# Performance work log

Hardware: AMD Instinct MI355X
Metric: run time of the kernel (lower is better)

## Reference

```python
import jax, jax.numpy as jnp
import numpy as np
import math

VOCAB = 32000
D = 256          # d_model
SLOTS = 128      # num_slots
RANK = 32        # bilinear_rank
STEPS = 6        # max_reasoning_steps
SEQ = 512
B = 4
LN_EPS = 1e-5


def _layernorm(x, gamma, beta):
    mu = jnp.mean(x, axis=-1, keepdims=True)
    var = jnp.var(x, axis=-1, keepdims=True)
    return (x - mu) * jax.lax.rsqrt(var + LN_EPS) * gamma + beta


def setup_inputs() -> dict:
    key = jax.random.key(0)
    ks = jax.random.split(key, 16)
    # orthogonal slots H: Q,_ = qr(randn(d, num_slots)); H = Q.T  (num_slots <= d_model)
    rng = np.random.RandomState(0)
    Q, _ = np.linalg.qr(rng.randn(D, SLOTS).astype(np.float32))
    H = jnp.asarray(Q.T)  # [SLOTS, D]

    input_ids = jax.random.randint(ks[0], (B, SEQ), 0, VOCAB)
    attention_mask = jnp.ones((B, SEQ), dtype=jnp.int32)

    tok_emb = jax.random.normal(ks[1], (VOCAB, D), jnp.float32) * 0.02
    tok_emb = tok_emb.at[0].set(0.0)  # padding_idx=0
    pos_emb = jax.random.normal(ks[2], (SEQ, D), jnp.float32) * 0.02

    std_bi = math.sqrt(2.0 / (D + RANK))
    W_source = jax.random.normal(ks[3], (SLOTS, SLOTS, D, RANK), jnp.float32) * std_bi
    W_target = jax.random.normal(ks[4], (SLOTS, SLOTS, RANK, D), jnp.float32) * std_bi

    lim = math.sqrt(6.0 / (D + D))  # xavier_uniform for the square linears
    def lin(k):
        return jax.random.uniform(k, (D, D), jnp.float32, -lim, lim)  # torch Linear weight [out,in]
    wq_in, wk_slots, wv_in = lin(ks[5]), lin(ks[6]), lin(ks[7])
    wq_out, wk_fin, wv_fin = lin(ks[8]), lin(ks[9]), lin(ks[10])
    w_out = jax.random.normal(ks[11], (VOCAB, D), jnp.float32) * 0.02

    ln_gamma = jnp.ones((STEPS, D), jnp.float32)
    ln_beta = jnp.zeros((STEPS, D), jnp.float32)

    return {
        "input_ids": input_ids, "attention_mask": attention_mask,
        "tok_emb": tok_emb, "pos_emb": pos_emb, "H": H,
        "W_source": W_source, "W_target": W_target,
        "wq_in": wq_in, "wk_slots": wk_slots, "wv_in": wv_in,
        "wq_out": wq_out, "wk_fin": wk_fin, "wv_fin": wv_fin,
        "w_out": w_out, "ln_gamma": ln_gamma, "ln_beta": ln_beta,
    }


def reference(input_ids, attention_mask, tok_emb, pos_emb, H, W_source, W_target,
              wq_in, wk_slots, wv_in, wq_out, wk_fin, wv_fin, w_out,
              ln_gamma, ln_beta):
    scale = 1.0 / math.sqrt(D)
    x = tok_emb[input_ids] + pos_emb[None, :input_ids.shape[1], :]  # [B,S,D] (dropout = eval no-op)

    # input -> slot compression cross-attention
    Qi = x @ wq_in.T                     # [B,S,D]
    K_slots = H @ wk_slots.T             # [SLOTS,D]
    Vi = x @ wv_in.T                     # [B,S,D]
    A = jax.nn.softmax(jnp.einsum('bsd,kd->bsk', Qi, K_slots) * scale, axis=-1)
    m = attention_mask[:, :, None].astype(A.dtype)
    A = A * m
    A = A / (A.sum(axis=1, keepdims=True) + 1e-8)
    IR = jnp.einsum('bsk,bsd->bkd', A, Vi)    # [B,SLOTS,D]
    Hs = H[None] + IR                          # [B,SLOTS,D]

    # bilinear all-pairs slot mixing, i != j, fused as one batched contraction
    pair_mask = 1.0 - jnp.eye(SLOTS, dtype=Hs.dtype)  # [SLOTS,SLOTS]
    for step in range(STEPS):
        inter = jnp.einsum('bid,ijdr->bijr', Hs, W_source) * pair_mask[None, :, :, None]
        influence = jnp.einsum('bijr,ijrd->bjd', inter, W_target)  # [B,SLOTS,D]
        Hs = Hs + jax.nn.relu(influence)
        Hs = _layernorm(Hs, ln_gamma[step], ln_beta[step])
        # convergence break omitted: step_update norms never fall below 0.01 with these scales

    # slot -> output expansion cross-attention
    Qo = x @ wq_out.T                          # [B,S,D]
    Kf = Hs @ wk_fin.T                         # [B,SLOTS,D]
    Vf = Hs @ wv_fin.T                         # [B,SLOTS,D]
    Ae = jax.nn.softmax(jnp.einsum('bsd,bkd->bsk', Qo, Kf) * scale, axis=-1)
    Y = jnp.einsum('bsk,bkd->bsd', Ae, Vf)
    logits = Y @ w_out.T                       # [B,S,VOCAB]
    return logits
```

## Files before the change

### kernel.cpp

```cpp
#include <hip/hip_runtime.h>

typedef unsigned short u16;
typedef unsigned long long u64;
typedef short short8_t __attribute__((ext_vector_type(8)));
typedef float f32x4 __attribute__((ext_vector_type(4)));

#define SL 128
#define DM 256
#define RK 32
#define SEQ 512
#define NB 4
#define NCHUNK 32

__device__ __forceinline__ float bf2f(u16 u) {
  return __uint_as_float(((unsigned int)u) << 16);
}
__device__ __forceinline__ u16 f2bf(float f) {
  unsigned int x = __float_as_uint(f);
  x += 0x7fffu + ((x >> 16) & 1u);
  return (u16)(x >> 16);
}

__global__ __launch_bounds__(256) void cvt_k(const float* __restrict__ in,
                                             u16* __restrict__ out, int n4) {
  for (int i = blockIdx.x * blockDim.x + threadIdx.x; i < n4;
       i += gridDim.x * blockDim.x) {
    float4 v = ((const float4*)in)[i];
    u16 o0 = f2bf(v.x), o1 = f2bf(v.y), o2 = f2bf(v.z), o3 = f2bf(v.w);
    unsigned int lo = (unsigned int)o0 | ((unsigned int)o1 << 16);
    unsigned int hi = (unsigned int)o2 | ((unsigned int)o3 << 16);
    ((uint2*)out)[i] = make_uint2(lo, hi);
  }
}

struct CvtJobs { const float* src[7]; };
__global__ __launch_bounds__(256) void cvt_all_k(CvtJobs jobs,
    u16* __restrict__ wbase, u16* __restrict__ Hbf) {
  int z = blockIdx.y;
  const float* in = jobs.src[z];
  u16* out = (z < 6) ? (wbase + (size_t)z * 65536) : Hbf;
  int n4 = (z < 6) ? 16384 : 8192;
  for (int i = blockIdx.x * 256 + threadIdx.x; i < n4; i += gridDim.x * 256) {
    float4 v = ((const float4*)in)[i];
    unsigned int lo = (unsigned)f2bf(v.x) | ((unsigned)f2bf(v.y) << 16);
    unsigned int hi = (unsigned)f2bf(v.z) | ((unsigned)f2bf(v.w) << 16);
    ((uint2*)out)[i] = make_uint2(lo, hi);
  }
}

__global__ __launch_bounds__(256) void embed_k(const int* __restrict__ ids,
    const float* __restrict__ tok, const float* __restrict__ pos,
    u16* __restrict__ xbf) {
  int bs = blockIdx.x, d = threadIdx.x;
  int id = ids[bs];
  int s = bs & (SEQ - 1);
  float v = tok[(size_t)id * DM + d] + pos[(size_t)s * DM + d];
  xbf[(size_t)bs * DM + d] = f2bf(v);
}

__global__ __launch_bounds__(256) void gemm_nt(const u16* __restrict__ A,
    const u16* __restrict__ Bw, float* __restrict__ Cout, int N) {
  __shared__ u16 s_a[64 * 256];
  __shared__ u16 s_b[64 * 256];
  int tid = threadIdx.x;
  int m0 = blockIdx.x * 64, n0 = blockIdx.y * 64;
  for (int c = tid; c < 2048; c += 256) {
    int row = c >> 5;
    int ec = (c & 31) << 3;
    short8_t va = *(const short8_t*)(A + (size_t)(m0 + row) * 256 + ec);
    short8_t vb = *(const short8_t*)(Bw + (size_t)(n0 + row) * 256 + ec);
    int sw = ec ^ ((row & 7) << 3);
    *(short8_t*)(&s_a[row * 256 + sw]) = va;
    *(short8_t*)(&s_b[row * 256 + sw]) = vb;
  }
  __syncthreads();
  int lane = tid & 63;
  int w = tid >> 6;
  int wm = (w >> 1) * 32, wn = (w & 1) * 32;
  int lr = lane & 15, lk = (lane >> 4) << 3;
  f32x4 acc00 = {0.f, 0.f, 0.f, 0.f};
  f32x4 acc01 = {0.f, 0.f, 0.f, 0.f};
  f32x4 acc10 = {0.f, 0.f, 0.f, 0.f};
  f32x4 acc11 = {0.f, 0.f, 0.f, 0.f};
#pragma unroll
  for (int ks = 0; ks < 8; ++ks) {
    int ke = ks * 32 + lk;
    int r0 = wm + lr, r1 = wm + 16 + lr;
    int c0 = wn + lr, c1 = wn + 16 + lr;
    short8_t a0 = *(const short8_t*)(&s_a[r0 * 256 + (ke ^ ((r0 & 7) << 3))]);
    short8_t a1 = *(const short8_t*)(&s_a[r1 * 256 + (ke ^ ((r1 & 7) << 3))]);
    short8_t b0 = *(const short8_t*)(&s_b[c0 * 256 + (ke ^ ((c0 & 7) << 3))]);
    short8_t b1 = *(const short8_t*)(&s_b[c1 * 256 + (ke ^ ((c1 & 7) << 3))]);
    acc00 = __builtin_amdgcn_mfma_f32_16x16x32_bf16(a0, b0, acc00, 0, 0, 0);
    acc01 = __builtin_amdgcn_mfma_f32_16x16x32_bf16(a0, b1, acc01, 0, 0, 0);
    acc10 = __builtin_amdgcn_mfma_f32_16x16x32_bf16(a1, b0, acc10, 0, 0, 0);
    acc11 = __builtin_amdgcn_mfma_f32_16x16x32_bf16(a1, b1, acc11, 0, 0, 0);
  }
  int rbase = (lane >> 4) << 2;
#pragma unroll
  for (int i = 0; i < 2; ++i) {
#pragma unroll
    for (int jj = 0; jj < 2; ++jj) {
      f32x4 v = (i == 0) ? (jj == 0 ? acc00 : acc01)
                         : (jj == 0 ? acc10 : acc11);
      int row0 = m0 + wm + i * 16 + rbase;
      int col = n0 + wn + jj * 16 + lr;
#pragma unroll
      for (int q = 0; q < 4; ++q)
        Cout[(size_t)(row0 + q) * (size_t)N + col] = v[q];
    }
  }
}

__global__ __launch_bounds__(256) void gemm_nt3(const u16* __restrict__ A,
    const u16* __restrict__ wbase, float* __restrict__ Cbase, int q0, int q1,
    int q2, size_t cstride) {
  int z = blockIdx.z;
  int q = (z == 0) ? q0 : ((z == 1) ? q1 : q2);
  const u16* Bw = wbase + (size_t)q * 65536;
  float* Cout = Cbase + (size_t)z * cstride;
  __shared__ u16 s_a[64 * 256];
  __shared__ u16 s_b[64 * 256];
  int tid = threadIdx.x;
  int m0 = blockIdx.x * 64, n0 = blockIdx.y * 64;
  for (int c = tid; c < 2048; c += 256) {
    int row = c >> 5;
    int ec = (c & 31) << 3;
    short8_t va = *(const short8_t*)(A + (size_t)(m0 + row) * 256 + ec);
    short8_t vb = *(const short8_t*)(Bw + (size_t)(n0 + row) * 256 + ec);
    int sw = ec ^ ((row & 7) << 3);
    *(short8_t*)(&s_a[row * 256 + sw]) = va;
    *(short8_t*)(&s_b[row * 256 + sw]) = vb;
  }
  __syncthreads();
  int lane = tid & 63;
  int w = tid >> 6;
  int wm = (w >> 1) * 32, wn = (w & 1) * 32;
  int lr = lane & 15, lk = (lane >> 4) << 3;
  f32x4 acc00 = {0.f, 0.f, 0.f, 0.f};
  f32x4 acc01 = {0.f, 0.f, 0.f, 0.f};
  f32x4 acc10 = {0.f, 0.f, 0.f, 0.f};
  f32x4 acc11 = {0.f, 0.f, 0.f, 0.f};
#pragma unroll
  for (int ks = 0; ks < 8; ++ks) {
    int ke = ks * 32 + lk;
    int r0 = wm + lr, r1 = wm + 16 + lr;
    int c0 = wn + lr, c1 = wn + 16 + lr;
    short8_t a0 = *(const short8_t*)(&s_a[r0 * 256 + (ke ^ ((r0 & 7) << 3))]);
    short8_t a1 = *(const short8_t*)(&s_a[r1 * 256 + (ke ^ ((r1 & 7) << 3))]);
    short8_t b0 = *(const short8_t*)(&s_b[c0 * 256 + (ke ^ ((c0 & 7) << 3))]);
    short8_t b1 = *(const short8_t*)(&s_b[c1 * 256 + (ke ^ ((c1 & 7) << 3))]);
    acc00 = __builtin_amdgcn_mfma_f32_16x16x32_bf16(a0, b0, acc00, 0, 0, 0);
    acc01 = __builtin_amdgcn_mfma_f32_16x16x32_bf16(a0, b1, acc01, 0, 0, 0);
    acc10 = __builtin_amdgcn_mfma_f32_16x16x32_bf16(a1, b0, acc10, 0, 0, 0);
    acc11 = __builtin_amdgcn_mfma_f32_16x16x32_bf16(a1, b1, acc11, 0, 0, 0);
  }
  int rbase = (lane >> 4) << 2;
#pragma unroll
  for (int i = 0; i < 2; ++i) {
#pragma unroll
    for (int jj = 0; jj < 2; ++jj) {
      f32x4 v = (i == 0) ? (jj == 0 ? acc00 : acc01)
                         : (jj == 0 ? acc10 : acc11);
      int row0 = m0 + wm + i * 16 + rbase;
      int col = n0 + wn + jj * 16 + lr;
#pragma unroll
      for (int q = 0; q < 4; ++q)
        Cout[(size_t)(row0 + q) * 256 + col] = v[q];
    }
  }
}

__global__ __launch_bounds__(512) void gemm128(const u16* __restrict__ A,
    const u16* __restrict__ Bw, float* __restrict__ Cout, int N) {
  __shared__ u16 s_a[128 * 128];
  __shared__ u16 s_b[128 * 128];
  int tid = threadIdx.x;
  int n0 = blockIdx.x * 128, m0 = blockIdx.y * 128;
  int lane = tid & 63, w = tid >> 6;
  int wm = (w >> 1) * 32;
  int wn = (w & 1) * 64;
  int lr = lane & 15, lk = (lane >> 4) << 3;
  f32x4 acc[2][4];
#pragma unroll
  for (int i = 0; i < 2; ++i)
#pragma unroll
    for (int t = 0; t < 4; ++t) acc[i][t] = {0.f, 0.f, 0.f, 0.f};
#pragma unroll
  for (int kc = 0; kc < 2; ++kc) {
    if (kc) __syncthreads();
    for (int c = tid; c < 2048; c += 512) {
      int row = c >> 4;
      int ec = (c & 15) << 3;
      short8_t va =
          *(const short8_t*)(A + (size_t)(m0 + row) * 256 + kc * 128 + ec);
      short8_t vb =
          *(const short8_t*)(Bw + (size_t)(n0 + row) * 256 + kc * 128 + ec);
      int sw = ec ^ ((row & 7) << 3);
      *(short8_t*)(&s_a[row * 128 + sw]) = va;
      *(short8_t*)(&s_b[row * 128 + sw]) = vb;
    }
    __syncthreads();
#pragma unroll
    for (int ks = 0; ks < 4; ++ks) {
      int ke = ks * 32 + lk;
      int r0 = wm + lr, r1 = wm + 16 + lr;
      short8_t a0 =
          *(const short8_t*)(&s_a[r0 * 128 + (ke ^ ((r0 & 7) << 3))]);
      short8_t a1 =
          *(const short8_t*)(&s_a[r1 * 128 + (ke ^ ((r1 & 7) << 3))]);
#pragma unroll
      for (int t = 0; t < 4; ++t) {
        int c0 = wn + t * 16 + lr;
        short8_t b0 =
            *(const short8_t*)(&s_b[c0 * 128 + (ke ^ ((c0 & 7) << 3))]);
        acc[0][t] = __builtin_amdgcn_mfma_f32_16x16x32_bf16(a0, b0, acc[0][t], 0, 0, 0);
        acc[1][t] = __builtin_amdgcn_mfma_f32_16x16x32_bf16(a1, b0, acc[1][t], 0, 0, 0);
      }
    }
  }
  int rbase = (lane >> 4) << 2;
#pragma unroll
  for (int i = 0; i < 2; ++i) {
#pragma unroll
    for (int t = 0; t < 4; ++t) {
      int row0 = m0 + wm + i * 16 + rbase;
      int col = n0 + wn + t * 16 + lr;
#pragma unroll
      for (int q = 0; q < 4; ++q)
        __builtin_nontemporal_store(acc[i][t][q],
                                    &Cout[(size_t)(row0 + q) * (size_t)N + col]);
    }
  }
}

__global__ __launch_bounds__(128) void attn_in_k(const float* __restrict__ Qi,
    const float* __restrict__ Ksl, const int* __restrict__ am,
    float* __restrict__ Aout) {
  int bs = blockIdx.x, t = threadIdx.x;
  __shared__ float s_q[DM];
  __shared__ float sred[2];
  s_q[t] = Qi[(size_t)bs * DM + t];
  s_q[t + 128] = Qi[(size_t)bs * DM + t + 128];
  __syncthreads();
  const float* kr = Ksl + (size_t)t * DM;
  float sc = 0.f;
#pragma unroll 8
  for (int d = 0; d < DM; ++d) sc += s_q[d] * kr[d];
  sc *= 0.0625f;
  float mx = sc;
#pragma unroll
  for (int m = 1; m < 64; m <<= 1) mx = fmaxf(mx, __shfl_xor(mx, m));
  if ((t & 63) == 0) sred[t >> 6] = mx;
  __syncthreads();
  mx = fmaxf(sred[0], sred[1]);
  float p = expf(sc - mx);
  float sum = p;
#pragma unroll
  for (int m = 1; m < 64; m <<= 1) sum += __shfl_xor(sum, m);
  __syncthreads();
  if ((t & 63) == 0) sred[t >> 6] = sum;
  __syncthreads();
  sum = sred[0] + sred[1];
  p = (p / sum) * (float)am[bs];
  Aout[(size_t)bs * SL + t] = p;
}

__global__ __launch_bounds__(512) void colsum_k(const float* __restrict__ A,
                                                float* __restrict__ dpart) {
  int t = threadIdx.x;
  int b = t >> 7, k = t & (SL - 1);
  int s0 = blockIdx.x * 32;
  const float* ap = A + (size_t)b * SEQ * SL + (size_t)s0 * SL + k;
  float s = 0.f;
#pragma unroll 4
  for (int si = 0; si < 32; ++si) s += ap[(size_t)si * SL];
  dpart[blockIdx.x * 512 + t] = s;
}

__global__ __launch_bounds__(256) void irhs_k(const float* __restrict__ A,
    const float* __restrict__ Vi, const float* __restrict__ dpart,
    const float* __restrict__ H, float* __restrict__ Hs) {
  int k = blockIdx.x, b = blockIdx.y, d = threadIdx.x;
  float den = 1e-8f;
#pragma unroll
  for (int i = 0; i < 16; ++i) den += dpart[i * 512 + b * SL + k];
  const float* ap = A + (size_t)b * SEQ * SL + k;
  const float* vp = Vi + (size_t)b * SEQ * DM + d;
  float s = 0.f;
#pragma unroll 4
  for (int si = 0; si < SEQ; ++si)
    s += ap[(size_t)si * SL] * vp[(size_t)si * DM];
  Hs[((size_t)b * SL + k) * DM + d] = H[(size_t)k * DM + d] + s / den;
}

template <int MODE>
__global__ __launch_bounds__(256, 2) void bilinear_k(
    const float* __restrict__ Hs, const void* __restrict__ Wsv,
    const void* __restrict__ Wtv, u16* __restrict__ Wsb,
    u16* __restrict__ Wtb, float* __restrict__ part) {
  constexpr int QN = (MODE == 0) ? 8 : 4;
  int j = blockIdx.x, ic = blockIdx.y, tid = threadIdx.x;
  int wv = tid >> 6, ln = tid & 63;
  __shared__ float s_hs[NB][4][DM];
  __shared__ float s_int[4][NB][RK];
  __shared__ float s_acc[4][NB][DM];
  int i0 = ic * 4;
  for (int c = tid; c < (NB * 4 * DM) / 4; c += 256) {
    int fi = c * 4;
    int b = fi >> 10, rest = fi & 1023;
    *(float4*)(&s_hs[0][0][0] + fi) =
        *(const float4*)(Hs + (size_t)b * SL * DM + (size_t)i0 * DM + rest);
  }
  __syncthreads();
  int il = wv;
  int i = i0 + il;
  float iacc[NB][QN];
#pragma unroll
  for (int b = 0; b < NB; ++b)
#pragma unroll
    for (int q = 0; q < QN; ++q) iacc[b][q] = 0.f;
  if (i != j) {
    size_t slab = (size_t)(i * SL + j) * (DM * RK);
    if constexpr (MODE == 0) {
      const u16* wp = (const u16*)Wsv + slab;
      const u16* tp = (const u16*)Wtv + slab;
      short8_t wsr[16], wtr[16];
#pragma unroll
      for (int t = 0; t < 16; ++t)
        wsr[t] = __builtin_nontemporal_load(
            (const short8_t*)(wp + t * 512 + ln * 8));
#pragma unroll
      for (int t = 0; t < 16; ++t)
        wtr[t] = __builtin_nontemporal_load(
            (const short8_t*)(tp + t * 512 + ln * 8));
      float racc[NB][8];
#pragma unroll
      for (int b = 0; b < NB; ++b)
#pragma unroll
        for (int q = 0; q < 8; ++q) racc[b][q] = 0.f;
#pragma unroll
      for (int t = 0; t < 16; ++t) {
        int d = t * 16 + (ln >> 2);
        float h0 = s_hs[0][il][d], h1 = s_hs[1][il][d];
        float h2 = s_hs[2][il][d], h3 = s_hs[3][il][d];
#pragma unroll
        for (int q = 0; q < 8; ++q) {
          float wf = bf2f((u16)wsr[t][q]);
          racc[0][q] += h0 * wf;
          racc[1][q] += h1 * wf;
          racc[2][q] += h2 * wf;
          racc[3][q] += h3 * wf;
        }
      }
#pragma unroll
      for (int m = 4; m <= 32; m <<= 1)
#pragma unroll
        for (int b = 0; b < NB; ++b)
#pragma unroll
          for (int q = 0; q < 8; ++q) racc[b][q] += __shfl_xor(racc[b][q], m);
      if ((ln >> 2) == 0) {
        int r0 = (ln & 3) * 8;
#pragma unroll
        for (int b = 0; b < NB; ++b)
#pragma unroll
          for (int q = 0; q < 8; ++q) s_int[wv][b][r0 + q] = racc[b][q];
      }
#pragma unroll
      for (int t = 0; t < 16; ++t) {
        int r = t * 2 + (ln >> 5);
        float v0 = s_int[wv][0][r], v1 = s_int[wv][1][r];
        float v2 = s_int[wv][2][r], v3 = s_int[wv][3][r];
#pragma unroll
        for (int q = 0; q < 8; ++q) {
          float wf = bf2f((u16)wtr[t][q]);
          iacc[0][q] += v0 * wf;
          iacc[1][q] += v1 * wf;
          iacc[2][q] += v2 * wf;
          iacc[3][q] += v3 * wf;
        }
      }
    } else {
      const float* wp = (const float*)Wsv + slab;
      const float* tp = (const float*)Wtv + slab;
      f32x4 wsr[32];
#pragma unroll
      for (int t = 0; t < 32; ++t)
        wsr[t] =
            __builtin_nontemporal_load((const f32x4*)(wp + t * 256 + ln * 4));
      float racc[NB][4];
#pragma unroll
      for (int b = 0; b < NB; ++b)
#pragma unroll
        for (int q = 0; q < 4; ++q) racc[b][q] = 0.f;
#pragma unroll
      for (int t = 0; t < 32; ++t) {
        f32x4 w4 = wsr[t];
        int d = t * 8 + (ln >> 3);
        float h0 = s_hs[0][il][d], h1 = s_hs[1][il][d];
        float h2 = s_hs[2][il][d], h3 = s_hs[3][il][d];
        racc[0][0] += h0 * w4[0]; racc[0][1] += h0 * w4[1];
        racc[0][2] += h0 * w4[2]; racc[0][3] += h0 * w4[3];
        racc[1][0] += h1 * w4[0]; racc[1][1] += h1 * w4[1];
        racc[1][2] += h1 * w4[2]; racc[1][3] += h1 * w4[3];
        racc[2][0] += h2 * w4[0]; racc[2][1] += h2 * w4[1];
        racc[2][2] += h2 * w4[2]; racc[2][3] += h2 * w4[3];
        racc[3][0] += h3 * w4[0]; racc[3][1] += h3 * w4[1];
        racc[3][2] += h3 * w4[2]; racc[3][3] += h3 * w4[3];
        if constexpr (MODE == 1) {
          u64 pk = (u64)((unsigned)f2bf(w4[0]) | ((unsigned)f2bf(w4[1]) << 16)) |
                   ((u64)((unsigned)f2bf(w4[2]) | ((unsigned)f2bf(w4[3]) << 16))
                    << 32);
          __builtin_nontemporal_store(pk, (u64*)(Wsb + slab + t * 256 + ln * 4));
        }
      }
#pragma unroll
      for (int m = 8; m <= 32; m <<= 1)
#pragma unroll
        for (int b = 0; b < NB; ++b)
#pragma unroll
          for (int q = 0; q < 4; ++q) racc[b][q] += __shfl_xor(racc[b][q], m);
      if ((ln >> 3) == 0) {
        int r0 = (ln & 7) * 4;
#pragma unroll
        for (int b = 0; b < NB; ++b)
#pragma unroll
          for (int q = 0; q < 4; ++q) s_int[wv][b][r0 + q] = racc[b][q];
      }
#pragma unroll
      for (int c8 = 0; c8 < 4; ++c8) {
        f32x4 wtr[8];
#pragma unroll
        for (int t = 0; t < 8; ++t)
          wtr[t] = __builtin_nontemporal_load(
              (const f32x4*)(tp + (c8 * 8 + t) * 256 + ln * 4));
#pragma unroll
        for (int t = 0; t < 8; ++t) {
          int r = c8 * 8 + t;
          f32x4 w4 = wtr[t];
          float v0 = s_int[wv][0][r], v1 = s_int[wv][1][r];
          float v2 = s_int[wv][2][r], v3 = s_int[wv][3][r];
          iacc[0][0] += v0 * w4[0]; iacc[0][1] += v0 * w4[1];
          iacc[0][2] += v0 * w4[2]; iacc[0][3] += v0 * w4[3];
          iacc[1][0] += v1 * w4[0]; iacc[1][1] += v1 * w4[1];
          iacc[1][2] += v1 * w4[2]; iacc[1][3] += v1 * w4[3];
          iacc[2][0] += v2 * w4[0]; iacc[2][1] += v2 * w4[1];
          iacc[2][2] += v2 * w4[2]; iacc[2][3] += v2 * w4[3];
          iacc[3][0] += v3 * w4[0]; iacc[3][1] += v3 * w4[1];
          iacc[3][2] += v3 * w4[2]; iacc[3][3] += v3 * w4[3];
          if constexpr (MODE == 1) {
            u64 pk =
                (u64)((unsigned)f2bf(w4[0]) | ((unsigned)f2bf(w4[1]) << 16)) |
                ((u64)((unsigned)f2bf(w4[2]) | ((unsigned)f2bf(w4[3]) << 16))
                 << 32);
            __builtin_nontemporal_store(pk,
                                        (u64*)(Wtb + slab + r * 256 + ln * 4));
          }
        }
      }
    }
  }
  if constexpr (MODE == 0) {
#pragma unroll
    for (int b = 0; b < NB; ++b)
#pragma unroll
      for (int q = 0; q < 8; ++q) iacc[b][q] += __shfl_xor(iacc[b][q], 32);
    if (ln < 32) {
#pragma unroll
      for (int b = 0; b < NB; ++b)
#pragma unroll
        for (int q = 0; q < 8; ++q) s_acc[wv][b][ln * 8 + q] = iacc[b][q];
    }
  } else {
#pragma unroll
    for (int b = 0; b < NB; ++b)
#pragma unroll
      for (int q = 0; q < 4; ++q) s_acc[wv][b][ln * 4 + q] = iacc[b][q];
  }
  __syncthreads();
  for (int c = tid; c < NB * DM; c += 256) {
    int b = c >> 8, d = c & 255;
    float s = s_acc[0][b][d] + s_acc[1][b][d] + s_acc[2][b][d] + s_acc[3][b][d];
    part[(((size_t)ic * NB + b) * SL + j) * DM + d] = s;
  }
}

__global__ __launch_bounds__(256) void ln_k(float* __restrict__ Hs,
    const float* __restrict__ part, const float* __restrict__ g,
    const float* __restrict__ be, int last, u16* __restrict__ Hs_bf) {
  int j = blockIdx.x, b = blockIdx.y, d = threadIdx.x;
  size_t base = ((size_t)b * SL + j) * DM + d;
  float inf = 0.f;
#pragma unroll
  for (int icc = 0; icc < NCHUNK; ++icc)
    inf += part[(((size_t)icc * NB + b) * SL + j) * DM + d];
  float h = Hs[base] + fmaxf(inf, 0.f);
  float s1 = h, s2 = h * h;
#pragma unroll
  for (int m = 1; m < 64; m <<= 1) {
    s1 += __shfl_xor(s1, m);
    s2 += __shfl_xor(s2, m);
  }
  __shared__ float r1[4], r2[4];
  int wv = d >> 6;
  if ((d & 63) == 0) { r1[wv] = s1; r2[wv] = s2; }
  __syncthreads();
  s1 = r1[0] + r1[1] + r1[2] + r1[3];
  s2 = r2[0] + r2[1] + r2[2] + r2[3];
  float mu = s1 * (1.f / 256.f);
  float var = s2 * (1.f / 256.f) - mu * mu;
  float o = (h - mu) * rsqrtf(var + 1e-5f) * g[d] + be[d];
  Hs[base] = o;
  if (last) Hs_bf[base] = f2bf(o);
}

__global__ __launch_bounds__(128) void attn_out_k(const float* __restrict__ Qo,
    const float* __restrict__ Kf, const float* __restrict__ Vf,
    u16* __restrict__ Ybf) {
  int bs = blockIdx.x, t = threadIdx.x;
  int b = bs >> 9;
  __shared__ float s_q[DM];
  __shared__ float s_p[SL];
  __shared__ float sred[2];
  s_q[t] = Qo[(size_t)bs * DM + t];
  s_q[t + 128] = Qo[(size_t)bs * DM + t + 128];
  __syncthreads();
  const float* kr = Kf + ((size_t)b * SL + t) * DM;
  float sc = 0.f;
#pragma unroll 8
  for (int d = 0; d < DM; ++d) sc += s_q[d] * kr[d];
  sc *= 0.0625f;
  float mx = sc;
#pragma unroll
  for (int m = 1; m < 64; m <<= 1) mx = fmaxf(mx, __shfl_xor(mx, m));
  if ((t & 63) == 0) sred[t >> 6] = mx;
  __syncthreads();
  mx = fmaxf(sred[0], sred[1]);
  float p = expf(sc - mx);
  float sum = p;
#pragma unroll
  for (int m = 1; m < 64; m <<= 1) sum += __shfl_xor(sum, m);
  __syncthreads();
  if ((t & 63) == 0) sred[t >> 6] = sum;
  __syncthreads();
  sum = sred[0] + sred[1];
  s_p[t] = p / sum;
  __syncthreads();
  for (int dd = t; dd < DM; dd += 128) {
    float y = 0.f;
    const float* vp = Vf + (size_t)b * SL * DM + dd;
#pragma unroll 8
    for (int k2 = 0; k2 < SL; ++k2) y += s_p[k2] * vp[(size_t)k2 * DM];
    Ybf[(size_t)bs * DM + dd] = f2bf(y);
  }
}

extern "C" void kernel_launch(void* const* d_in, const int* in_sizes, int n_in,
                              void* d_out, int out_size, void* d_ws,
                              size_t ws_size, hipStream_t stream) {
  (void)in_sizes; (void)n_in; (void)out_size;
  const int* ids = (const int*)d_in[0];
  const int* amask = (const int*)d_in[1];
  const float* tok = (const float*)d_in[2];
  const float* pos = (const float*)d_in[3];
  const float* Hsl = (const float*)d_in[4];
  const float* Ws = (const float*)d_in[5];
  const float* Wt = (const float*)d_in[6];
  const float* wq_in = (const float*)d_in[7];
  const float* wk_sl = (const float*)d_in[8];
  const float* wv_in = (const float*)d_in[9];
  const float* wq_out = (const float*)d_in[10];
  const float* wk_fin = (const float*)d_in[11];
  const float* wv_fin = (const float*)d_in[12];
  const float* w_out = (const float*)d_in[13];
  const float* lng = (const float*)d_in[14];
  const float* lnb = (const float*)d_in[15];

  char* base = (char*)d_ws;
  size_t used = 0;
  auto carve = [&](size_t bytes) {
    void* r = base + used;
    used += (bytes + 255) & ~(size_t)255;
    return r;
  };
  u16* x_bf = (u16*)carve((size_t)2048 * 256 * 2);
  float* Qi = (float*)carve((size_t)2048 * 256 * 4);
  float* Vi = (float*)carve((size_t)2048 * 256 * 4);
  float* Qo = (float*)carve((size_t)2048 * 256 * 4);
  float* Ksl = (float*)carve((size_t)128 * 256 * 4);
  float* Aat = (float*)carve((size_t)4 * 512 * 128 * 4);
  float* dpart = (float*)carve((size_t)16 * 512 * 4);
  float* Hst = (float*)carve((size_t)4 * 128 * 256 * 4);
  u16* Hs_bf = (u16*)carve((size_t)4 * 128 * 256 * 2);
  float* part = (float*)carve((size_t)NCHUNK * 4 * 128 * 256 * 4);
  float* Kf = (float*)carve((size_t)4 * 128 * 256 * 4);
  float* Vf = (float*)carve((size_t)4 * 128 * 256 * 4);
  u16* Ybf = (u16*)carve((size_t)2048 * 256 * 2);
  u16* wbase = (u16*)carve((size_t)6 * 65536 * 2);
  u16* Hbf = (u16*)carve((size_t)128 * 256 * 2);
  u16* w_out_bf = (u16*)carve((size_t)32000 * 256 * 2);
  const size_t WN = (size_t)128 * 128 * 256 * 32;
  bool bigws = (used + 2 * WN * 2 + 512) <= ws_size;
  u16* Ws_bf = nullptr;
  u16* Wt_bf = nullptr;
  if (bigws) {
    Ws_bf = (u16*)carve(WN * 2);
    Wt_bf = (u16*)carve(WN * 2);
  }

  CvtJobs cj;
  cj.src[0] = wq_in; cj.src[1] = wk_sl; cj.src[2] = wv_in;
  cj.src[3] = wq_out; cj.src[4] = wk_fin; cj.src[5] = wv_fin;
  cj.src[6] = Hsl;
  cvt_all_k<<<dim3(64, 7), 256, 0, stream>>>(cj, wbase, Hbf);
  cvt_k<<<2048, 256, 0, stream>>>(w_out, w_out_bf, (int)(32000 * 256 / 4));

  embed_k<<<2048, 256, 0, stream>>>(ids, tok, pos, x_bf);
  gemm_nt3<<<dim3(32, 4, 3), 256, 0, stream>>>(x_bf, wbase, Qi, 0, 2, 3,
                                               (size_t)2048 * 256);
  gemm_nt<<<dim3(2, 4), 256, 0, stream>>>(Hbf, wbase + (size_t)1 * 65536, Ksl,
                                          256);
  attn_in_k<<<2048, 128, 0, stream>>>(Qi, Ksl, amask, Aat);
  colsum_k<<<16, 512, 0, stream>>>(Aat, dpart);
  irhs_k<<<dim3(128, 4), 256, 0, stream>>>(Aat, Vi, dpart, Hsl, Hst);
  for (int step = 0; step < 6; ++step) {
    if (bigws) {
      if (step == 0)
        bilinear_k<1><<<dim3(SL, 32), 256, 0, stream>>>(Hst, Ws, Wt, Ws_bf,
                                                        Wt_bf, part);
      else
        bilinear_k<0><<<dim3(SL, 32), 256, 0, stream>>>(Hst, Ws_bf, Wt_bf,
                                                        nullptr, nullptr, part);
    } else {
      bilinear_k<2><<<dim3(SL, 32), 256, 0, stream>>>(Hst, Ws, Wt, nullptr,
                                                      nullptr, part);
    }
    ln_k<<<dim3(128, 4), 256, 0, stream>>>(Hst, part, lng + step * DM,
                                           lnb + step * DM, step == 5 ? 1 : 0,
                                           Hs_bf);
  }
  gemm_nt3<<<dim3(8, 4, 2), 256, 0, stream>>>(Hs_bf, wbase, Kf, 4, 5, 5,
                                              (size_t)4 * 128 * 256);
  attn_out_k<<<2048, 128, 0, stream>>>(Qo, Kf, Vf, Ybf);
  gemm128<<<dim3(250, 16), 512, 0, stream>>>(Ybf, w_out_bf, (float*)d_out,
                                             32000);
}
```

Baseline: 1.010 ms.

## Process eight source slots per wave in bilinear kernel with double-buffered weight loads

The bilinear kernel now has each wave loop over 8 source slots (i) instead of 1, cutting the grid from 32 to 4 i-chunks and the partial-sum count (NCHUNK) from 32 to 4. In the bf16 mode the next slot's W_source slab is prefetched into a second register buffer while the current slot is computed, and packed f32x2 math is used to encourage dual-issue FMAs. Hs is read straight from global memory instead of being staged in LDS. The aim is better latency hiding and less partial-sum traffic for ln_k, at the cost of far fewer blocks (512) and higher register pressure, which may lower occupancy.

Result: slower. 1.603 ms (+58.8%).

```diff
diff --git a/kernel.cpp b/kernel.cpp
--- a/kernel.cpp
+++ b/kernel.cpp
@@ -1,16 +1,18 @@
 #include <hip/hip_runtime.h>
 
 typedef unsigned short u16;
+typedef unsigned int u32;
 typedef unsigned long long u64;
 typedef short short8_t __attribute__((ext_vector_type(8)));
 typedef float f32x4 __attribute__((ext_vector_type(4)));
+typedef float f32x2 __attribute__((ext_vector_type(2)));
 
 #define SL 128
 #define DM 256
 #define RK 32
 #define SEQ 512
 #define NB 4
-#define NCHUNK 32
+#define NCHUNK 4
 
 __device__ __forceinline__ float bf2f(u16 u) {
   return __uint_as_float(((unsigned int)u) << 16);
@@ -19,6 +21,12 @@
   unsigned int x = __float_as_uint(f);
   x += 0x7fffu + ((x >> 16) & 1u);
   return (u16)(x >> 16);
+}
+__device__ __forceinline__ f32x2 bfpair(u32 u) {
+  f32x2 r;
+  r[0] = __uint_as_float(u << 16);
+  r[1] = __uint_as_float(u & 0xffff0000u);
+  return r;
 }
 
 __global__ __launch_bounds__(256) void cvt_k(const float* __restrict__ in,
@@ -26,9 +34,8 @@
   for (int i = blockIdx.x * blockDim.x + threadIdx.x; i < n4;
        i += gridDim.x * blockDim.x) {
     float4 v = ((const float4*)in)[i];
-    u16 o0 = f2bf(v.x), o1 = f2bf(v.y), o2 = f2bf(v.z), o3 = f2bf(v.w);
-    unsigned int lo = (unsigned int)o0 | ((unsigned int)o1 << 16);
-    unsigned int hi = (unsigned int)o2 | ((unsigned int)o3 << 16);
+    unsigned int lo = (unsigned)f2bf(v.x) | ((unsigned)f2bf(v.y) << 16);
+    unsigned int hi = (unsigned)f2bf(v.z) | ((unsigned)f2bf(v.w) << 16);
     ((uint2*)out)[i] = make_uint2(lo, hi);
   }
 }
@@ -299,95 +306,147 @@
     const float* __restrict__ Hs, const void* __restrict__ Wsv,
     const void* __restrict__ Wtv, u16* __restrict__ Wsb,
     u16* __restrict__ Wtb, float* __restrict__ part) {
-  constexpr int QN = (MODE == 0) ? 8 : 4;
   int j = blockIdx.x, ic = blockIdx.y, tid = threadIdx.x;
   int wv = tid >> 6, ln = tid & 63;
-  __shared__ float s_hs[NB][4][DM];
   __shared__ float s_int[4][NB][RK];
   __shared__ float s_acc[4][NB][DM];
-  int i0 = ic * 4;
-  for (int c = tid; c < (NB * 4 * DM) / 4; c += 256) {
-    int fi = c * 4;
-    int b = fi >> 10, rest = fi & 1023;
-    *(float4*)(&s_hs[0][0][0] + fi) =
-        *(const float4*)(Hs + (size_t)b * SL * DM + (size_t)i0 * DM + rest);
-  }
-  __syncthreads();
-  int il = wv;
-  int i = i0 + il;
-  float iacc[NB][QN];
-#pragma unroll
-  for (int b = 0; b < NB; ++b)
-#pragma unroll
-    for (int q = 0; q < QN; ++q) iacc[b][q] = 0.f;
-  if (i != j) {
-    size_t slab = (size_t)(i * SL + j) * (DM * RK);
-    if constexpr (MODE == 0) {
-      const u16* wp = (const u16*)Wsv + slab;
-      const u16* tp = (const u16*)Wtv + slab;
-      short8_t wsr[16], wtr[16];
+  int ibase = ic * 32 + wv * 8;
+
+  if constexpr (MODE == 0) {
+    const u16* Wsp = (const u16*)Wsv;
+    const u16* Wtp = (const u16*)Wtv;
+    f32x2 iacc[NB][4];
+#pragma unroll
+    for (int b = 0; b < NB; ++b)
+#pragma unroll
+      for (int q = 0; q < 4; ++q) iacc[b][q] = {0.f, 0.f};
+    short8_t ws[2][16];
+    {
+      size_t slab0 = (size_t)(ibase * SL + j) * (DM * RK);
 #pragma unroll
       for (int t = 0; t < 16; ++t)
-        wsr[t] = __builtin_nontemporal_load(
-            (const short8_t*)(wp + t * 512 + ln * 8));
+        ws[0][t] = __builtin_nontemporal_load(
+            (const short8_t*)(Wsp + slab0 + t * 512 + ln * 8));
+      __builtin_amdgcn_sched_barrier(0);
+    }
+#pragma unroll
+    for (int p = 0; p < 8; ++p) {
+      int cur = p & 1;
+      int i = ibase + p;
+      size_t slab = (size_t)(i * SL + j) * (DM * RK);
+      short8_t wt[16];
 #pragma unroll
       for (int t = 0; t < 16; ++t)
-        wtr[t] = __builtin_nontemporal_load(
-            (const short8_t*)(tp + t * 512 + ln * 8));
-      float racc[NB][8];
+        wt[t] = __builtin_nontemporal_load(
+            (const short8_t*)(Wtp + slab + t * 512 + ln * 8));
+      __builtin_amdgcn_sched_barrier(0);
+      f32x2 racc[NB][4];
 #pragma unroll
       for (int b = 0; b < NB; ++b)
 #pragma unroll
-        for (int q = 0; q < 8; ++q) racc[b][q] = 0.f;
+        for (int q = 0; q < 4; ++q) racc[b][q] = {0.f, 0.f};
 #pragma unroll
       for (int t = 0; t < 16; ++t) {
         int d = t * 16 + (ln >> 2);
-        float h0 = s_hs[0][il][d], h1 = s_hs[1][il][d];
-        float h2 = s_hs[2][il][d], h3 = s_hs[3][il][d];
-#pragma unroll
-        for (int q = 0; q < 8; ++q) {
-          float wf = bf2f((u16)wsr[t][q]);
-          racc[0][q] += h0 * wf;
-          racc[1][q] += h1 * wf;
-          racc[2][q] += h2 * wf;
-          racc[3][q] += h3 * wf;
-        }
-      }
-#pragma unroll
-      for (int m = 4; m <= 32; m <<= 1)
-#pragma unroll
-        for (int b = 0; b < NB; ++b)
-#pragma unroll
-          for (int q = 0; q < 8; ++q) racc[b][q] += __shfl_xor(racc[b][q], m);
-      if ((ln >> 2) == 0) {
-        int r0 = (ln & 3) * 8;
-#pragma unroll
-        for (int b = 0; b < NB; ++b)
-#pragma unroll
-          for (int q = 0; q < 8; ++q) s_int[wv][b][r0 + q] = racc[b][q];
-      }
-#pragma unroll
-      for (int t = 0; t < 16; ++t) {
-        int r = t * 2 + (ln >> 5);
-        float v0 = s_int[wv][0][r], v1 = s_int[wv][1][r];
-        float v2 = s_int[wv][2][r], v3 = s_int[wv][3][r];
-#pragma unroll
-        for (int q = 0; q < 8; ++q) {
-          float wf = bf2f((u16)wtr[t][q]);
-          iacc[0][q] += v0 * wf;
-          iacc[1][q] += v1 * wf;
-          iacc[2][q] += v2 * wf;
-          iacc[3][q] += v3 * wf;
-        }
-      }
-    } else {
-      const float* wp = (const float*)Wsv + slab;
-      const float* tp = (const float*)Wtv + slab;
+        uint4 wu = *(const uint4*)(&ws[cur][t]);
+        f32x2 w0 = bfpair(wu.x), w1 = bfpair(wu.y);
+        f32x2 w2 = bfpair(wu.z), w3 = bfpair(wu.w);
+#pragma unroll
+        for (int b = 0; b < NB; ++b) {
+          float h = Hs[((size_t)b * SL + i) * DM + d];
+          f32x2 h2 = {h, h};
+          racc[b][0] += h2 * w0;
+          racc[b][1] += h2 * w1;
+          racc[b][2] += h2 * w2;
+          racc[b][3] += h2 * w3;
+        }
+      }
+      if (p < 7) {
+        size_t slabn = (size_t)((i + 1) * SL + j) * (DM * RK);
+#pragma unroll
+        for (int t = 0; t < 16; ++t)
+          ws[cur ^ 1][t] = __builtin_nontemporal_load(
+              (const short8_t*)(Wsp + slabn + t * 512 + ln * 8));
+        __builtin_amdgcn_sched_barrier(0);
+      }
+      if (i != j) {
+#pragma unroll
+        for (int m = 4; m <= 32; m <<= 1)
+#pragma unroll
+          for (int b = 0; b < NB; ++b)
+#pragma unroll
+            for (int q = 0; q < 4; ++q) {
+              f32x2 o;
+              o[0] = __shfl_xor(racc[b][q][0], m);
+              o[1] = __shfl_xor(racc[b][q][1], m);
+              racc[b][q] += o;
+            }
+        if ((ln >> 2) == 0) {
+          int r0 = (ln & 3) * 8;
+#pragma unroll
+          for (int b = 0; b < NB; ++b)
+#pragma unroll
+            for (int q = 0; q < 4; ++q) {
+              s_int[wv][b][r0 + q * 2] = racc[b][q][0];
+              s_int[wv][b][r0 + q * 2 + 1] = racc[b][q][1];
+            }
+        }
+#pragma unroll
+        for (int t = 0; t < 16; ++t) {
+          int r = t * 2 + (ln >> 5);
+          uint4 wu = *(const uint4*)(&wt[t]);
+          f32x2 w0 = bfpair(wu.x), w1 = bfpair(wu.y);
+          f32x2 w2 = bfpair(wu.z), w3 = bfpair(wu.w);
+#pragma unroll
+          for (int b = 0; b < NB; ++b) {
+            float v = s_int[wv][b][r];
+            f32x2 v2 = {v, v};
+            iacc[b][0] += v2 * w0;
+            iacc[b][1] += v2 * w1;
+            iacc[b][2] += v2 * w2;
+            iacc[b][3] += v2 * w3;
+          }
+        }
+      }
+    }
+#pragma unroll
+    for (int b = 0; b < NB; ++b)
+#pragma unroll
+      for (int q = 0; q < 4; ++q) {
+        f32x2 o;
+        o[0] = __shfl_xor(iacc[b][q][0], 32);
+        o[1] = __shfl_xor(iacc[b][q][1], 32);
+        iacc[b][q] += o;
+      }
+    if (ln < 32) {
+#pragma unroll
+      for (int b = 0; b < NB; ++b)
+#pragma unroll
+        for (int q = 0; q < 4; ++q) {
+          s_acc[wv][b][ln * 8 + q * 2] = iacc[b][q][0];
+          s_acc[wv][b][ln * 8 + q * 2 + 1] = iacc[b][q][1];
+        }
+    }
+  } else {
+    const float* Wsp = (const float*)Wsv;
+    const float* Wtp = (const float*)Wtv;
+    float iacc[NB][4];
+#pragma unroll
+    for (int b = 0; b < NB; ++b)
+#pragma unroll
+      for (int q = 0; q < 4; ++q) iacc[b][q] = 0.f;
+#pragma unroll 1
+    for (int p = 0; p < 8; ++p) {
+      int i = ibase + p;
+      size_t slab = (size_t)(i * SL + j) * (DM * RK);
+      const float* wp = Wsp + slab;
+      const float* tp = Wtp + slab;
       f32x4 wsr[32];
 #pragma unroll
       for (int t = 0; t < 32; ++t)
         wsr[t] =
             __builtin_nontemporal_load((const f32x4*)(wp + t * 256 + ln * 4));
+      __builtin_amdgcn_sched_barrier(0);
       float racc[NB][4];
 #pragma unroll
       for (int b = 0; b < NB; ++b)
@@ -397,16 +456,14 @@
       for (int t = 0; t < 32; ++t) {
         f32x4 w4 = wsr[t];
         int d = t * 8 + (ln >> 3);
-        float h0 = s_hs[0][il][d], h1 = s_hs[1][il][d];
-        float h2 = s_hs[2][il][d], h3 = s_hs[3][il][d];
-        racc[0][0] += h0 * w4[0]; racc[0][1] += h0 * w4[1];
-        racc[0][2] += h0 * w4[2]; racc[0][3] += h0 * w4[3];
-        racc[1][0] += h1 * w4[0]; racc[1][1] += h1 * w4[1];
-        racc[1][2] += h1 * w4[2]; racc[1][3] += h1 * w4[3];
-        racc[2][0] += h2 * w4[0]; racc[2][1] += h2 * w4[1];
-        racc[2][2] += h2 * w4[2]; racc[2][3] += h2 * w4[3];
-        racc[3][0] += h3 * w4[0]; racc[3][1] += h3 * w4[1];
-        racc[3][2] += h3 * w4[2]; racc[3][3] += h3 * w4[3];
+#pragma unroll
+        for (int b = 0; b < NB; ++b) {
+          float h = Hs[((size_t)b * SL + i) * DM + d];
+          racc[b][0] += h * w4[0];
+          racc[b][1] += h * w4[1];
+          racc[b][2] += h * w4[2];
+          racc[b][3] += h * w4[3];
+        }
         if constexpr (MODE == 1) {
           u64 pk = (u64)((unsigned)f2bf(w4[0]) | ((unsigned)f2bf(w4[1]) << 16)) |
                    ((u64)((unsigned)f2bf(w4[2]) | ((unsigned)f2bf(w4[3]) << 16))
@@ -414,18 +471,20 @@
           __builtin_nontemporal_store(pk, (u64*)(Wsb + slab + t * 256 + ln * 4));
         }
       }
-#pragma unroll
-      for (int m = 8; m <= 32; m <<= 1)
-#pragma unroll
-        for (int b = 0; b < NB; ++b)
-#pragma unroll
-          for (int q = 0; q < 4; ++q) racc[b][q] += __shfl_xor(racc[b][q], m);
-      if ((ln >> 3) == 0) {
-        int r0 = (ln & 7) * 4;
-#pragma unroll
-        for (int b = 0; b < NB; ++b)
-#pragma unroll
-          for (int q = 0; q < 4; ++q) s_int[wv][b][r0 + q] = racc[b][q];
+      if (i != j) {
+#pragma unroll
+        for (int m = 8; m <= 32; m <<= 1)
+#pragma unroll
+          for (int b = 0; b < NB; ++b)
+#pragma unroll
+            for (int q = 0; q < 4; ++q) racc[b][q] += __shfl_xor(racc[b][q], m);
+        if ((ln >> 3) == 0) {
+          int r0 = (ln & 7) * 4;
+#pragma unroll
+          for (int b = 0; b < NB; ++b)
+#pragma unroll
+            for (int q = 0; q < 4; ++q) s_int[wv][b][r0 + q] = racc[b][q];
+        }
       }
 #pragma unroll
       for (int c8 = 0; c8 < 4; ++c8) {
@@ -434,20 +493,11 @@
         for (int t = 0; t < 8; ++t)
           wtr[t] = __builtin_nontemporal_load(
               (const f32x4*)(tp + (c8 * 8 + t) * 256 + ln * 4));
+        __builtin_amdgcn_sched_barrier(0);
 #pragma unroll
         for (int t = 0; t < 8; ++t) {
           int r = c8 * 8 + t;
           f32x4 w4 = wtr[t];
-          float v0 = s_int[wv][0][r], v1 = s_int[wv][1][r];
-          float v2 = s_int[wv][2][r], v3 = s_int[wv][3][r];
-          iacc[0][0] += v0 * w4[0]; iacc[0][1] += v0 * w4[1];
-          iacc[0][2] += v0 * w4[2]; iacc[0][3] += v0 * w4[3];
-          iacc[1][0] += v1 * w4[0]; iacc[1][1] += v1 * w4[1];
-          iacc[1][2] += v1 * w4[2]; iacc[1][3] += v1 * w4[3];
-          iacc[2][0] += v2 * w4[0]; iacc[2][1] += v2 * w4[1];
-          iacc[2][2] += v2 * w4[2]; iacc[2][3] += v2 * w4[3];
-          iacc[3][0] += v3 * w4[0]; iacc[3][1] += v3 * w4[1];
-          iacc[3][2] += v3 * w4[2]; iacc[3][3] += v3 * w4[3];
           if constexpr (MODE == 1) {
             u64 pk =
                 (u64)((unsigned)f2bf(w4[0]) | ((unsigned)f2bf(w4[1]) << 16)) |
@@ -456,22 +506,21 @@
             __builtin_nontemporal_store(pk,
                                         (u64*)(Wtb + slab + r * 256 + ln * 4));
           }
-        }
-      }
-    }
-  }
-  if constexpr (MODE == 0) {
-#pragma unroll
-    for (int b = 0; b < NB; ++b)
-#pragma unroll
-      for (int q = 0; q < 8; ++q) iacc[b][q] += __shfl_xor(iacc[b][q], 32);
-    if (ln < 32) {
-#pragma unroll
-      for (int b = 0; b < NB; ++b)
-#pragma unroll
-        for (int q = 0; q < 8; ++q) s_acc[wv][b][ln * 8 + q] = iacc[b][q];
-    }
-  } else {
+          if (i != j) {
+            float v0 = s_int[wv][0][r], v1 = s_int[wv][1][r];
+            float v2 = s_int[wv][2][r], v3 = s_int[wv][3][r];
+            iacc[0][0] += v0 * w4[0]; iacc[0][1] += v0 * w4[1];
+            iacc[0][2] += v0 * w4[2]; iacc[0][3] += v0 * w4[3];
+            iacc[1][0] += v1 * w4[0]; iacc[1][1] += v1 * w4[1];
+            iacc[1][2] += v1 * w4[2]; iacc[1][3] += v1 * w4[3];
+            iacc[2][0] += v2 * w4[0]; iacc[2][1] += v2 * w4[1];
+            iacc[2][2] += v2 * w4[2]; iacc[2][3] += v2 * w4[3];
+            iacc[3][0] += v3 * w4[0]; iacc[3][1] += v3 * w4[1];
+            iacc[3][2] += v3 * w4[2]; iacc[3][3] += v3 * w4[3];
+          }
+        }
+      }
+    }
 #pragma unroll
     for (int b = 0; b < NB; ++b)
 #pragma unroll
@@ -626,14 +675,14 @@
   for (int step = 0; step < 6; ++step) {
     if (bigws) {
       if (step == 0)
-        bilinear_k<1><<<dim3(SL, 32), 256, 0, stream>>>(Hst, Ws, Wt, Ws_bf,
-                                                        Wt_bf, part);
+        bilinear_k<1><<<dim3(SL, 4), 256, 0, stream>>>(Hst, Ws, Wt, Ws_bf,
+                                                       Wt_bf, part);
       else
-        bilinear_k<0><<<dim3(SL, 32), 256, 0, stream>>>(Hst, Ws_bf, Wt_bf,
-                                                        nullptr, nullptr, part);
+        bilinear_k<0><<<dim3(SL, 4), 256, 0, stream>>>(Hst, Ws_bf, Wt_bf,
+                                                       nullptr, nullptr, part);
     } else {
-      bilinear_k<2><<<dim3(SL, 32), 256, 0, stream>>>(Hst, Ws, Wt, nullptr,
-                                                      nullptr, part);
+      bilinear_k<2><<<dim3(SL, 4), 256, 0, stream>>>(Hst, Ws, Wt, nullptr,
+                                                     nullptr, part);
     }
     ln_k<<<dim3(128, 4), 256, 0, stream>>>(Hst, part, lng + step * DM,
                                            lnb + step * DM, step == 5 ? 1 : 0,
```

## Process four source slots per wave in bilinear kernel, cut chunk count

Applied to the files above, without the earlier changes.

Each wave in the bilinear slot-mixing kernel now loops over four source slots i instead of one, and the i-chunk grid dimension drops from 32 to 8. That means partial sums accumulate in registers across slots, and fewer partials are written and later reduced by the layernorm pass. The shared-memory staging of Hs is removed, so Hs values are read directly from global memory (L1/L2 cached). The occupancy hint in launch_bounds is dropped. In exchange the grid is four times smaller (1024 blocks) and the loop over slots is serial, which risks less latency hiding for the weight streaming, which dominates the cost.

After: 1.029 ms. Within noise of the previous version (+2.0%).

```diff
diff --git a/kernel.cpp b/kernel.cpp
--- a/kernel.cpp
+++ b/kernel.cpp
@@ -1,6 +1,7 @@
 #include <hip/hip_runtime.h>
 
 typedef unsigned short u16;
+typedef unsigned int u32;
 typedef unsigned long long u64;
 typedef short short8_t __attribute__((ext_vector_type(8)));
 typedef float f32x4 __attribute__((ext_vector_type(4)));
@@ -10,7 +11,7 @@
 #define RK 32
 #define SEQ 512
 #define NB 4
-#define NCHUNK 32
+#define NCHUNK 8
 
 __device__ __forceinline__ float bf2f(u16 u) {
   return __uint_as_float(((unsigned int)u) << 16);
@@ -26,9 +27,8 @@
   for (int i = blockIdx.x * blockDim.x + threadIdx.x; i < n4;
        i += gridDim.x * blockDim.x) {
     float4 v = ((const float4*)in)[i];
-    u16 o0 = f2bf(v.x), o1 = f2bf(v.y), o2 = f2bf(v.z), o3 = f2bf(v.w);
-    unsigned int lo = (unsigned int)o0 | ((unsigned int)o1 << 16);
-    unsigned int hi = (unsigned int)o2 | ((unsigned int)o3 << 16);
+    unsigned int lo = (unsigned)f2bf(v.x) | ((unsigned)f2bf(v.y) << 16);
+    unsigned int hi = (unsigned)f2bf(v.z) | ((unsigned)f2bf(v.w) << 16);
     ((uint2*)out)[i] = make_uint2(lo, hi);
   }
 }
@@ -295,36 +295,31 @@
 }
 
 template <int MODE>
-__global__ __launch_bounds__(256, 2) void bilinear_k(
+__global__ __launch_bounds__(256) void bilinear_k(
     const float* __restrict__ Hs, const void* __restrict__ Wsv,
     const void* __restrict__ Wtv, u16* __restrict__ Wsb,
     u16* __restrict__ Wtb, float* __restrict__ part) {
-  constexpr int QN = (MODE == 0) ? 8 : 4;
   int j = blockIdx.x, ic = blockIdx.y, tid = threadIdx.x;
   int wv = tid >> 6, ln = tid & 63;
-  __shared__ float s_hs[NB][4][DM];
   __shared__ float s_int[4][NB][RK];
   __shared__ float s_acc[4][NB][DM];
-  int i0 = ic * 4;
-  for (int c = tid; c < (NB * 4 * DM) / 4; c += 256) {
-    int fi = c * 4;
-    int b = fi >> 10, rest = fi & 1023;
-    *(float4*)(&s_hs[0][0][0] + fi) =
-        *(const float4*)(Hs + (size_t)b * SL * DM + (size_t)i0 * DM + rest);
-  }
-  __syncthreads();
-  int il = wv;
-  int i = i0 + il;
-  float iacc[NB][QN];
-#pragma unroll
-  for (int b = 0; b < NB; ++b)
-#pragma unroll
-    for (int q = 0; q < QN; ++q) iacc[b][q] = 0.f;
-  if (i != j) {
-    size_t slab = (size_t)(i * SL + j) * (DM * RK);
-    if constexpr (MODE == 0) {
-      const u16* wp = (const u16*)Wsv + slab;
-      const u16* tp = (const u16*)Wtv + slab;
+  int ibase = ic * 16 + wv * 4;
+
+  if constexpr (MODE == 0) {
+    const u16* Wsp = (const u16*)Wsv;
+    const u16* Wtp = (const u16*)Wtv;
+    float iacc[NB][8];
+#pragma unroll
+    for (int b = 0; b < NB; ++b)
+#pragma unroll
+      for (int q = 0; q < 8; ++q) iacc[b][q] = 0.f;
+#pragma unroll 1
+    for (int p = 0; p < 4; ++p) {
+      int i = ibase + p;
+      if (i == j) continue;
+      size_t slab = (size_t)(i * SL + j) * (DM * RK);
+      const u16* wp = Wsp + slab;
+      const u16* tp = Wtp + slab;
       short8_t wsr[16], wtr[16];
 #pragma unroll
       for (int t = 0; t < 16; ++t)
@@ -342,8 +337,10 @@
 #pragma unroll
       for (int t = 0; t < 16; ++t) {
         int d = t * 16 + (ln >> 2);
-        float h0 = s_hs[0][il][d], h1 = s_hs[1][il][d];
-        float h2 = s_hs[2][il][d], h3 = s_hs[3][il][d];
+        float h0 = Hs[((size_t)0 * SL + i) * DM + d];
+        float h1 = Hs[((size_t)1 * SL + i) * DM + d];
+        float h2 = Hs[((size_t)2 * SL + i) * DM + d];
+        float h3 = Hs[((size_t)3 * SL + i) * DM + d];
 #pragma unroll
         for (int q = 0; q < 8; ++q) {
           float wf = bf2f((u16)wsr[t][q]);
@@ -380,52 +377,80 @@
           iacc[3][q] += v3 * wf;
         }
       }
-    } else {
-      const float* wp = (const float*)Wsv + slab;
-      const float* tp = (const float*)Wtv + slab;
-      f32x4 wsr[32];
-#pragma unroll
-      for (int t = 0; t < 32; ++t)
-        wsr[t] =
-            __builtin_nontemporal_load((const f32x4*)(wp + t * 256 + ln * 4));
+    }
+#pragma unroll
+    for (int b = 0; b < NB; ++b)
+#pragma unroll
+      for (int q = 0; q < 8; ++q) iacc[b][q] += __shfl_xor(iacc[b][q], 32);
+    if (ln < 32) {
+#pragma unroll
+      for (int b = 0; b < NB; ++b)
+#pragma unroll
+        for (int q = 0; q < 8; ++q) s_acc[wv][b][ln * 8 + q] = iacc[b][q];
+    }
+  } else {
+    const float* Wsp = (const float*)Wsv;
+    const float* Wtp = (const float*)Wtv;
+    float iacc[NB][4];
+#pragma unroll
+    for (int b = 0; b < NB; ++b)
+#pragma unroll
+      for (int q = 0; q < 4; ++q) iacc[b][q] = 0.f;
+#pragma unroll 1
+    for (int p = 0; p < 4; ++p) {
+      int i = ibase + p;
+      size_t slab = (size_t)(i * SL + j) * (DM * RK);
+      const float* wp = Wsp + slab;
+      const float* tp = Wtp + slab;
       float racc[NB][4];
 #pragma unroll
       for (int b = 0; b < NB; ++b)
 #pragma unroll
         for (int q = 0; q < 4; ++q) racc[b][q] = 0.f;
 #pragma unroll
-      for (int t = 0; t < 32; ++t) {
-        f32x4 w4 = wsr[t];
-        int d = t * 8 + (ln >> 3);
-        float h0 = s_hs[0][il][d], h1 = s_hs[1][il][d];
-        float h2 = s_hs[2][il][d], h3 = s_hs[3][il][d];
-        racc[0][0] += h0 * w4[0]; racc[0][1] += h0 * w4[1];
-        racc[0][2] += h0 * w4[2]; racc[0][3] += h0 * w4[3];
-        racc[1][0] += h1 * w4[0]; racc[1][1] += h1 * w4[1];
-        racc[1][2] += h1 * w4[2]; racc[1][3] += h1 * w4[3];
-        racc[2][0] += h2 * w4[0]; racc[2][1] += h2 * w4[1];
-        racc[2][2] += h2 * w4[2]; racc[2][3] += h2 * w4[3];
-        racc[3][0] += h3 * w4[0]; racc[3][1] += h3 * w4[1];
-        racc[3][2] += h3 * w4[2]; racc[3][3] += h3 * w4[3];
-        if constexpr (MODE == 1) {
-          u64 pk = (u64)((unsigned)f2bf(w4[0]) | ((unsigned)f2bf(w4[1]) << 16)) |
-                   ((u64)((unsigned)f2bf(w4[2]) | ((unsigned)f2bf(w4[3]) << 16))
-                    << 32);
-          __builtin_nontemporal_store(pk, (u64*)(Wsb + slab + t * 256 + ln * 4));
+      for (int c8 = 0; c8 < 4; ++c8) {
+        f32x4 wsr[8];
+#pragma unroll
+        for (int t = 0; t < 8; ++t)
+          wsr[t] = __builtin_nontemporal_load(
+              (const f32x4*)(wp + (c8 * 8 + t) * 256 + ln * 4));
+#pragma unroll
+        for (int t = 0; t < 8; ++t) {
+          int tt = c8 * 8 + t;
+          f32x4 w4 = wsr[t];
+          int d = tt * 8 + (ln >> 3);
+#pragma unroll
+          for (int b = 0; b < NB; ++b) {
+            float h = Hs[((size_t)b * SL + i) * DM + d];
+            racc[b][0] += h * w4[0];
+            racc[b][1] += h * w4[1];
+            racc[b][2] += h * w4[2];
+            racc[b][3] += h * w4[3];
+          }
+          if constexpr (MODE == 1) {
+            u64 pk =
+                (u64)((unsigned)f2bf(w4[0]) | ((unsigned)f2bf(w4[1]) << 16)) |
+                ((u64)((unsigned)f2bf(w4[2]) | ((unsigned)f2bf(w4[3]) << 16))
+                 << 32);
+            __builtin_nontemporal_store(pk,
+                                        (u64*)(Wsb + slab + tt * 256 + ln * 4));
+          }
         }
       }
-#pragma unroll
-      for (int m = 8; m <= 32; m <<= 1)
-#pragma unroll
-        for (int b = 0; b < NB; ++b)
-#pragma unroll
-          for (int q = 0; q < 4; ++q) racc[b][q] += __shfl_xor(racc[b][q], m);
-      if ((ln >> 3) == 0) {
-        int r0 = (ln & 7) * 4;
-#pragma unroll
-        for (int b = 0; b < NB; ++b)
-#pragma unroll
-          for (int q = 0; q < 4; ++q) s_int[wv][b][r0 + q] = racc[b][q];
+      if (i != j) {
+#pragma unroll
+        for (int m = 8; m <= 32; m <<= 1)
+#pragma unroll
+          for (int b = 0; b < NB; ++b)
+#pragma unroll
+            for (int q = 0; q < 4; ++q) racc[b][q] += __shfl_xor(racc[b][q], m);
+        if ((ln >> 3) == 0) {
+          int r0 = (ln & 7) * 4;
+#pragma unroll
+          for (int b = 0; b < NB; ++b)
+#pragma unroll
+            for (int q = 0; q < 4; ++q) s_int[wv][b][r0 + q] = racc[b][q];
+        }
       }
 #pragma unroll
       for (int c8 = 0; c8 < 4; ++c8) {
@@ -438,16 +463,6 @@
         for (int t = 0; t < 8; ++t) {
           int r = c8 * 8 + t;
           f32x4 w4 = wtr[t];
-          float v0 = s_int[wv][0][r], v1 = s_int[wv][1][r];
-          float v2 = s_int[wv][2][r], v3 = s_int[wv][3][r];
-          iacc[0][0] += v0 * w4[0]; iacc[0][1] += v0 * w4[1];
-          iacc[0][2] += v0 * w4[2]; iacc[0][3] += v0 * w4[3];
-          iacc[1][0] += v1 * w4[0]; iacc[1][1] += v1 * w4[1];
-          iacc[1][2] += v1 * w4[2]; iacc[1][3] += v1 * w4[3];
-          iacc[2][0] += v2 * w4[0]; iacc[2][1] += v2 * w4[1];
-          iacc[2][2] += v2 * w4[2]; iacc[2][3] += v2 * w4[3];
-          iacc[3][0] += v3 * w4[0]; iacc[3][1] += v3 * w4[1];
-          iacc[3][2] += v3 * w4[2]; iacc[3][3] += v3 * w4[3];
           if constexpr (MODE == 1) {
             u64 pk =
                 (u64)((unsigned)f2bf(w4[0]) | ((unsigned)f2bf(w4[1]) << 16)) |
@@ -456,22 +471,21 @@
             __builtin_nontemporal_store(pk,
                                         (u64*)(Wtb + slab + r * 256 + ln * 4));
           }
+          if (i != j) {
+            float v0 = s_int[wv][0][r], v1 = s_int[wv][1][r];
+            float v2 = s_int[wv][2][r], v3 = s_int[wv][3][r];
+            iacc[0][0] += v0 * w4[0]; iacc[0][1] += v0 * w4[1];
+            iacc[0][2] += v0 * w4[2]; iacc[0][3] += v0 * w4[3];
+            iacc[1][0] += v1 * w4[0]; iacc[1][1] += v1 * w4[1];
+            iacc[1][2] += v1 * w4[2]; iacc[1][3] += v1 * w4[3];
+            iacc[2][0] += v2 * w4[0]; iacc[2][1] += v2 * w4[1];
+            iacc[2][2] += v2 * w4[2]; iacc[2][3] += v2 * w4[3];
+            iacc[3][0] += v3 * w4[0]; iacc[3][1] += v3 * w4[1];
+            iacc[3][2] += v3 * w4[2]; iacc[3][3] += v3 * w4[3];
+          }
         }
       }
     }
-  }
-  if constexpr (MODE == 0) {
-#pragma unroll
-    for (int b = 0; b < NB; ++b)
-#pragma unroll
-      for (int q = 0; q < 8; ++q) iacc[b][q] += __shfl_xor(iacc[b][q], 32);
-    if (ln < 32) {
-#pragma unroll
-      for (int b = 0; b < NB; ++b)
-#pragma unroll
-        for (int q = 0; q < 8; ++q) s_acc[wv][b][ln * 8 + q] = iacc[b][q];
-    }
-  } else {
 #pragma unroll
     for (int b = 0; b < NB; ++b)
 #pragma unroll
@@ -626,14 +640,14 @@
   for (int step = 0; step < 6; ++step) {
     if (bigws) {
       if (step == 0)
-        bilinear_k<1><<<dim3(SL, 32), 256, 0, stream>>>(Hst, Ws, Wt, Ws_bf,
-                                                        Wt_bf, part);
+        bilinear_k<1><<<dim3(SL, NCHUNK), 256, 0, stream>>>(Hst, Ws, Wt, Ws_bf,
+                                                            Wt_bf, part);
       else
-        bilinear_k<0><<<dim3(SL, 32), 256, 0, stream>>>(Hst, Ws_bf, Wt_bf,
-                                                        nullptr, nullptr, part);
+        bilinear_k<0><<<dim3(SL, NCHUNK), 256, 0, stream>>>(
+            Hst, Ws_bf, Wt_bf, nullptr, nullptr, part);
     } else {
-      bilinear_k<2><<<dim3(SL, 32), 256, 0, stream>>>(Hst, Ws, Wt, nullptr,
-                                                      nullptr, part);
+      bilinear_k<2><<<dim3(SL, NCHUNK), 256, 0, stream>>>(Hst, Ws, Wt, nullptr,
+                                                          nullptr, part);
     }
     ln_k<<<dim3(128, 4), 256, 0, stream>>>(Hst, part, lng + step * DM,
                                            lnb + step * DM, step == 5 ? 1 : 0,
```
